# Kernel tuning notes

Measured on AMD Instinct MI355X. Metric: run time of the kernel, lower is better.

The kernel has to match this reference:

```python
import jax, jax.numpy as jnp
import numpy as np

N_NODES = 20000
N_EDGES = 60000
N_GRAPHS = 512
TOWERS = 4
F_OUT_T = 18  # out_channels // towers
HID = 72      # 8 * 9
EPS_BN = 1e-5
EPS_STD = 1e-5
DEG_HIST = np.array([67167, 3157428, 5106064, 885236, 453935, 0, 11152], dtype=np.float64)
AVG_DEG_LOG = float((np.log(np.arange(7) + 1.0) * DEG_HIST).sum() / DEG_HIST.sum())
UNITSCALE = jnp.array([[[1.0, 1.0, 100.0, 0.01, 1000.0, 0.0, 1e-5]]], dtype=jnp.float32)


def _lin(key, fan_in, fan_out, prefix=()):
    kw, kb = jax.random.split(key)
    s = 1.0 / np.sqrt(fan_in)
    w = jax.random.uniform(kw, prefix + (fan_in, fan_out), jnp.float32, -s, s)
    b = jax.random.uniform(kb, prefix + (fan_out,), jnp.float32, -s, s)
    return w, b


def setup_inputs() -> dict:
    key = jax.random.key(0)
    ks = list(jax.random.split(key, 32))
    it = iter(ks)
    nk = lambda: next(it)
    inp = {}
    inp['x'] = jax.random.normal(nk(), (N_NODES, 9), jnp.float32)
    inp['edge_attr'] = jax.random.normal(nk(), (N_EDGES, 3), jnp.float32)
    inp['edge_index'] = jax.random.randint(nk(), (2, N_EDGES), 0, N_NODES, jnp.int32)
    inp['batch'] = jnp.sort(jax.random.randint(nk(), (N_NODES,), 0, N_GRAPHS, jnp.int32))
    # conv layer 0: F_in = 9
    inp['c0_ew'], inp['c0_eb'] = _lin(nk(), 3, 9)
    inp['c0_prw'], inp['c0_prb'] = _lin(nk(), 27, 9, (TOWERS,))      # pre: 3*F_in -> F_in
    inp['c0_pow'], inp['c0_pob'] = _lin(nk(), 117, 18, (TOWERS,))   # post: 13*F_in -> 18
    inp['c0_lw'], inp['c0_lb'] = _lin(nk(), HID, HID)
    inp['c0_g'] = jnp.ones((HID,), jnp.float32)
    inp['c0_be'] = jnp.zeros((HID,), jnp.float32)
    # conv layers 1-3 stacked: F_in = 72
    inp['cs_ew'], inp['cs_eb'] = _lin(nk(), 3, HID, (3,))
    inp['cs_prw'], inp['cs_prb'] = _lin(nk(), 216, HID, (3, TOWERS))
    inp['cs_pow'], inp['cs_pob'] = _lin(nk(), 936, 18, (3, TOWERS))
    inp['cs_lw'], inp['cs_lb'] = _lin(nk(), HID, HID, (3,))
    inp['cs_g'] = jnp.ones((3, HID), jnp.float32)
    inp['cs_be'] = jnp.zeros((3, HID), jnp.float32)
    # MLP heads
    for m, out_d in (('m1', 3), ('m2', 7), ('m3', 7)):
        inp[m + '_w1'], inp[m + '_b1'] = _lin(nk(), HID, 50)
        inp[m + '_g1'] = jnp.ones((50,), jnp.float32)
        inp[m + '_be1'] = jnp.zeros((50,), jnp.float32)
        inp[m + '_w2'], inp[m + '_b2'] = _lin(nk(), 50, 25)
        inp[m + '_g2'] = jnp.ones((25,), jnp.float32)
        inp[m + '_be2'] = jnp.zeros((25,), jnp.float32)
        inp[m + '_w3'], inp[m + '_b3'] = _lin(nk(), 25, out_d)
    return inp


def _batchnorm(x, g, b):
    # training-mode BatchNorm1d (biased variance)
    mu = x.mean(axis=0)
    var = x.var(axis=0)
    return (x - mu) * jax.lax.rsqrt(var + EPS_BN) * g + b


def _pna_conv(x, src, dst, edge_attr, ew, eb, prw, prb, pow_, pob, lw, lb):
    n, f_in = x.shape
    e_enc = edge_attr @ ew + eb                                 # [E, F_in]
    h = jnp.concatenate([x[dst], x[src], e_enc], axis=-1)       # [E, 3*F_in]
    # per-tower pre-MLP (pre_layers=1 -> single Linear); input identical per tower
    msg = jnp.einsum('ef,tfo->eto', h, prw) + prb               # [E, T, F_in]

    deg = jax.ops.segment_sum(jnp.ones((src.shape[0],), jnp.float32), dst, n)  # in-degree [N]
    degc = jnp.maximum(deg, 1.0)[:, None, None]
    s1 = jax.ops.segment_sum(msg, dst, n)
    s2 = jax.ops.segment_sum(msg * msg, dst, n)
    mean = s1 / degc
    var = jax.nn.relu(s2 / degc - mean * mean)
    std = jnp.sqrt(var + EPS_STD)
    has = (deg > 0)[:, None, None]
    mn = jnp.where(has, jax.ops.segment_min(msg, dst, n), 0.0)
    mx = jnp.where(has, jax.ops.segment_max(msg, dst, n), 0.0)
    agg = jnp.concatenate([mean, mn, mx, std], axis=-1)         # [N, T, 4*F_in]

    amp = (jnp.log(jnp.maximum(deg, 1.0) + 1.0) / AVG_DEG_LOG)[:, None, None]
    out = jnp.concatenate([agg, agg * amp, agg / amp], axis=-1)  # identity/amplification/attenuation

    xt = jnp.broadcast_to(x[:, None, :], (n, TOWERS, f_in))
    comb = jnp.concatenate([xt, out], axis=-1)                  # [N, T, 13*F_in]
    o = jnp.einsum('ntf,tfo->nto', comb, pow_) + pob            # [N, T, 18]
    return o.reshape(n, TOWERS * F_OUT_T) @ lw + lb             # [N, 72]


def _mlp_head(x, w1, b1, g1, be1, w2, b2, g2, be2, w3, b3):
    h = jax.nn.relu(_batchnorm(x @ w1 + b1, g1, be1))
    h = jax.nn.relu(_batchnorm(h @ w2 + b2, g2, be2))
    return h @ w3 + b3


def _forward(x, edge_attr, edge_index, batch,
             c0_ew, c0_eb, c0_prw, c0_prb, c0_pow, c0_pob, c0_lw, c0_lb, c0_g, c0_be,
             cs_ew, cs_eb, cs_prw, cs_prb, cs_pow, cs_pob, cs_lw, cs_lb, cs_g, cs_be,
             m1_w1, m1_b1, m1_g1, m1_be1, m1_w2, m1_b2, m1_g2, m1_be2, m1_w3, m1_b3,
             m2_w1, m2_b1, m2_g1, m2_be1, m2_w2, m2_b2, m2_g2, m2_be2, m2_w3, m2_b3,
             m3_w1, m3_b1, m3_g1, m3_be1, m3_w2, m3_b2, m3_g2, m3_be2, m3_w3, m3_b3):
    src, dst = edge_index[0], edge_index[1]
    h = _pna_conv(x, src, dst, edge_attr, c0_ew, c0_eb, c0_prw, c0_prb, c0_pow, c0_pob, c0_lw, c0_lb)
    h = jax.nn.relu(_batchnorm(h, c0_g, c0_be))
    for i in range(3):
        h = _pna_conv(h, src, dst, edge_attr, cs_ew[i], cs_eb[i], cs_prw[i], cs_prb[i],
                      cs_pow[i], cs_pob[i], cs_lw[i], cs_lb[i])
        h = jax.nn.relu(_batchnorm(h, cs_g[i], cs_be[i]))
    g = jax.ops.segment_sum(h, batch, N_GRAPHS)                 # global_add_pool -> [G, 72]
    kij = jnp.tanh(_mlp_head(g, m1_w1, m1_b1, m1_g1, m1_be1, m1_w2, m1_b2, m1_g2, m1_be2, m1_w3, m1_b3))
    kij = jnp.broadcast_to(kij[:, None, :], (N_GRAPHS, 2, 3))
    c1 = jax.nn.relu(_mlp_head(g, m2_w1, m2_b1, m2_g1, m2_be1, m2_w2, m2_b2, m2_g2, m2_be2, m2_w3, m2_b3))[:, None, :]
    c2 = jax.nn.relu(_mlp_head(g, m3_w1, m3_b1, m3_g1, m3_be1, m3_w2, m3_b2, m3_g2, m3_be2, m3_w3, m3_b3))[:, None, :]
    out = jnp.concatenate([c1, c2], axis=1) + UNITSCALE         # [G, 2, 7]
    return jnp.concatenate([out, kij], axis=-1)                 # [G, 2, 10]


def reference(x, edge_attr, edge_index, batch,
              c0_ew, c0_eb, c0_prw, c0_prb, c0_pow, c0_pob, c0_lw, c0_lb, c0_g, c0_be,
              cs_ew, cs_eb, cs_prw, cs_prb, cs_pow, cs_pob, cs_lw, cs_lb, cs_g, cs_be,
              m1_w1, m1_b1, m1_g1, m1_be1, m1_w2, m1_b2, m1_g2, m1_be2, m1_w3, m1_b3,
              m2_w1, m2_b1, m2_g1, m2_be1, m2_w2, m2_b2, m2_g2, m2_be2, m2_w3, m2_b3,
              m3_w1, m3_b1, m3_g1, m3_be1, m3_w2, m3_b2, m3_g2, m3_be2, m3_w3, m3_b3):
    return _forward(x, edge_attr, edge_index, batch,
                    c0_ew, c0_eb, c0_prw, c0_prb, c0_pow, c0_pob, c0_lw, c0_lb, c0_g, c0_be,
                    cs_ew, cs_eb, cs_prw, cs_prb, cs_pow, cs_pob, cs_lw, cs_lb, cs_g, cs_be,
                    m1_w1, m1_b1, m1_g1, m1_be1, m1_w2, m1_b2, m1_g2, m1_be2, m1_w3, m1_b3,
                    m2_w1, m2_b1, m2_g1, m2_be1, m2_w2, m2_b2, m2_g2, m2_be2, m2_w3, m2_b3,
                    m3_w1, m3_b1, m3_g1, m3_be1, m3_w2, m3_b2, m3_g2, m3_be2, m3_w3, m3_b3)
```

## Files before the change

kernel.cpp:

```cpp
#include <hip/hip_runtime.h>
#include <math.h>
#include <cstdint>

#define N_NODES 20000
#define N_EDGES 60000
#define N_GRAPHS 512
#define NT 4

__global__ void count_deg_k(const int* __restrict__ dst, int* __restrict__ deg) {
  int e = blockIdx.x * blockDim.x + threadIdx.x;
  if (e < N_EDGES) atomicAdd(&deg[dst[e]], 1);
}

__global__ void scan_rowptr_k(const int* __restrict__ deg, int* __restrict__ rp) {
  __shared__ int ss[1024];
  int tid = threadIdx.x;
  const int per = (N_NODES + 1023) / 1024;
  int base = tid * per;
  int s = 0;
  for (int i = 0; i < per; i++) { int idx = base + i; if (idx < N_NODES) s += deg[idx]; }
  ss[tid] = s;
  __syncthreads();
  for (int off = 1; off < 1024; off <<= 1) {
    int v = (tid >= off) ? ss[tid - off] : 0;
    __syncthreads();
    ss[tid] += v;
    __syncthreads();
  }
  int run = ss[tid] - s;
  for (int i = 0; i < per; i++) {
    int idx = base + i;
    if (idx < N_NODES) { rp[idx] = run; run += deg[idx]; }
  }
  if (tid == 0) rp[N_NODES] = ss[1023];
}

__global__ void fill_csr_k(const int* __restrict__ dst, const int* __restrict__ rp,
                           int* __restrict__ cur, int* __restrict__ eids) {
  int e = blockIdx.x * blockDim.x + threadIdx.x;
  if (e < N_EDGES) {
    int d = dst[e];
    int pos = atomicAdd(&cur[d], 1);
    eids[rp[d] + pos] = e;
  }
}

__global__ void amp_k(const int* __restrict__ deg, float* __restrict__ amp, float adl) {
  int n = blockIdx.x * blockDim.x + threadIdx.x;
  if (n < N_NODES) {
    float d = (float)(deg[n] > 0 ? deg[n] : 1);
    amp[n] = logf(d + 1.0f) / adl;
  }
}

__global__ void gboundary_k(const int* __restrict__ batch, int* __restrict__ grp) {
  int n = blockIdx.x * blockDim.x + threadIdx.x;
  if (n >= N_NODES) return;
  int bn = batch[n];
  int bp = (n == 0) ? -1 : batch[n - 1];
  for (int g = bp + 1; g <= bn; g++) grp[g] = n;
  if (n == N_NODES - 1)
    for (int g = bn + 1; g <= N_GRAPHS; g++) grp[g] = N_NODES;
}

template <int AVEC, int BNA, int EPI>
__global__ __launch_bounds__(256, 2) void sgemm2_k(
    const float* __restrict__ A, const float* __restrict__ B, float* __restrict__ C,
    const float* __restrict__ bias, int M, int N, int K, int lda, int ldb, int ldc,
    int nb, int ns, long long bsA, long long bsB,
    const float* __restrict__ vsc, const float* __restrict__ vsh,
    const float* __restrict__ amp, float* __restrict__ y0, int ldy,
    double* __restrict__ bnsums) {
  constexpr int SM = (EPI == 1) ? 128 * 57 : (16 * 128 + 16 * 64);
  __shared__ float smem[SM];
  float(*As)[128] = (float(*)[128])smem;
  float(*Bs)[64] = (float(*)[64])(smem + 16 * 128);

  const int tid = threadIdx.x;
  const int tx = tid & 15, ty = tid >> 4;
  const int m0 = blockIdx.x * 128, n0 = blockIdx.y * 64;
  const int z = blockIdx.z;
  A += bsA * z; B += bsB * z;

  float acc[8][4] = {};
  for (int k0 = 0; k0 < K; k0 += 16) {
    if (AVEC) {
#pragma unroll
      for (int it = 0; it < 2; ++it) {
        int u = it * 256 + tid;
        int row = u >> 2, q = u & 3;
        int gm = m0 + row, gk = k0 + 4 * q;
        float4 v = make_float4(0.f, 0.f, 0.f, 0.f);
        if (gm < M && gk < K) {
          v = *(const float4*)&A[(long long)gm * lda + gk];
          if (BNA) {
            float4 sc = *(const float4*)&vsc[gk];
            float4 sh = *(const float4*)&vsh[gk];
            v.x = fmaxf(v.x * sc.x + sh.x, 0.f);
            v.y = fmaxf(v.y * sc.y + sh.y, 0.f);
            v.z = fmaxf(v.z * sc.z + sh.z, 0.f);
            v.w = fmaxf(v.w * sc.w + sh.w, 0.f);
          }
        }
        As[4 * q + 0][row] = v.x;
        As[4 * q + 1][row] = v.y;
        As[4 * q + 2][row] = v.z;
        As[4 * q + 3][row] = v.w;
      }
    } else {
#pragma unroll
      for (int it = 0; it < 8; ++it) {
        int u = it * 256 + tid;
        int row = u >> 4, kk = u & 15;
        int gm = m0 + row, gk = k0 + kk;
        float v = 0.f;
        if (gm < M && gk < K) {
          v = A[(long long)gm * lda + gk];
          if (BNA) v = fmaxf(v * vsc[gk] + vsh[gk], 0.f);
        }
        As[kk][row] = v;
      }
    }
    {
      int kk = tid >> 4, n4 = (tid & 15) * 4;
      int gk = k0 + kk, gn = n0 + n4;
      float4 v = make_float4(0.f, 0.f, 0.f, 0.f);
      if (gk < K && gn < nb) v = *(const float4*)&B[(long long)gk * ldb + gn];
      *(float4*)&Bs[kk][n4] = v;
    }
    __syncthreads();
#pragma unroll
    for (int kk = 0; kk < 16; ++kk) {
      float a[8], b[4];
#pragma unroll
      for (int i = 0; i < 8; i++) a[i] = As[kk][ty * 8 + i];
#pragma unroll
      for (int j = 0; j < 4; j++) b[j] = Bs[kk][tx * 4 + j];
#pragma unroll
      for (int i = 0; i < 8; i++)
#pragma unroll
        for (int j = 0; j < 4; j++) acc[i][j] += a[i] * b[j];
    }
    __syncthreads();
  }

  if (EPI == 1) {
    float(*Ps)[57] = (float(*)[57])smem;
    int c0 = tx * 4;
#pragma unroll
    for (int i = 0; i < 8; i++) {
      if (c0 < 56) {
#pragma unroll
        for (int j = 0; j < 4; j++) Ps[ty * 8 + i][c0 + j] = acc[i][j];
      }
    }
    __syncthreads();
#pragma unroll
    for (int it = 0; it < 9; ++it) {
      int item = it * 256 + tid;
      int r = item / 18, o = item - r * 18;
      int gm = m0 + r;
      if (gm < M) {
        float a = amp[gm];
        float v = Ps[r][o] + a * Ps[r][18 + o] + Ps[r][36 + o] / a;
        y0[(long long)gm * ldy + z * 18 + o] += v;
      }
    }
    return;
  }

  int gn = n0 + tx * 4;
  float cs[4] = {0.f, 0.f, 0.f, 0.f}, cq[4] = {0.f, 0.f, 0.f, 0.f};
  if (gn < ns) {
    float b0 = 0.f, b1 = 0.f, b2 = 0.f, b3 = 0.f;
    if (bias) { b0 = bias[gn]; b1 = bias[gn + 1]; b2 = bias[gn + 2]; b3 = bias[gn + 3]; }
#pragma unroll
    for (int i = 0; i < 8; i++) {
      int gm = m0 + ty * 8 + i;
      if (gm >= M) continue;
      float4 v;
      v.x = acc[i][0] + b0; v.y = acc[i][1] + b1;
      v.z = acc[i][2] + b2; v.w = acc[i][3] + b3;
      *(float4*)&C[(long long)gm * ldc + gn] = v;
      if (EPI == 2) {
        cs[0] += v.x; cs[1] += v.y; cs[2] += v.z; cs[3] += v.w;
        cq[0] += v.x * v.x; cq[1] += v.y * v.y; cq[2] += v.z * v.z; cq[3] += v.w * v.w;
      }
    }
  }
  if (EPI == 2) {
    __syncthreads();
    float* psum = smem;
    float* psq = smem + 1024;
#pragma unroll
    for (int j = 0; j < 4; j++) {
      psum[ty * 64 + tx * 4 + j] = cs[j];
      psq[ty * 64 + tx * 4 + j] = cq[j];
    }
    __syncthreads();
    if (tid < 64) {
      float s = 0.f, q = 0.f;
#pragma unroll
      for (int t = 0; t < 16; t++) { s += psum[t * 64 + tid]; q += psq[t * 64 + tid]; }
      int gcol = n0 + tid;
      if (gcol < N) {
        atomicAdd(&bnsums[gcol], (double)s);
        atomicAdd(&bnsums[72 + gcol], (double)q);
      }
    }
  }
}

__global__ void agg_fused_k(const float* __restrict__ XdXs, int ldx, const float* __restrict__ ea,
                            const int* __restrict__ srcI, const int* __restrict__ rp,
                            const int* __restrict__ eids, const float* __restrict__ Wec,
                            const float* __restrict__ bec, float* __restrict__ agg, int F) {
  const int C = 4 * F;
  long long idx = (long long)blockIdx.x * blockDim.x + threadIdx.x;
  if (idx >= (long long)N_NODES * C) return;
  int n = (int)(idx / C), c = (int)(idx % C);
  int s = rp[n], e = rp[n + 1];
  float w0 = Wec[c], w1 = Wec[C + c], w2 = Wec[2 * C + c], bc = bec[c];
  float sum = 0.f, sq = 0.f, mn = INFINITY, mx = -INFINITY;
  for (int i = s; i < e; i++) {
    int eid = eids[i];
    int sr = srcI[eid];
    float v = XdXs[(long long)sr * ldx + C + c] + ea[eid * 3 + 0] * w0 +
              ea[eid * 3 + 1] * w1 + ea[eid * 3 + 2] * w2 + bc;
    sum += v; sq += v * v;
    mn = fminf(mn, v); mx = fmaxf(mx, v);
  }
  int t = c / F, f = c % F;
  long long base = (long long)n * 4 * C + (long long)t * 4 * F;
  float mean, stdv;
  if (e == s) {
    mean = 0.f; mn = 0.f; mx = 0.f; stdv = sqrtf(1e-5f);
  } else {
    float inv = 1.f / (float)(e - s);
    float xd = XdXs[(long long)n * ldx + c];
    float mu = sum * inv;
    float var = sq * inv - mu * mu;
    if (var < 0.f) var = 0.f;
    stdv = sqrtf(var + 1e-5f);
    mean = xd + mu; mn += xd; mx += xd;
  }
  agg[base + f] = mean;
  agg[base + F + f] = mn;
  agg[base + 2 * F + f] = mx;
  agg[base + 3 * F + f] = stdv;
}

__global__ void repack2_k(const float* __restrict__ prw, const float* __restrict__ pw,
                          const float* __restrict__ ew, const float* __restrict__ eb,
                          const float* __restrict__ prb, const float* __restrict__ pob,
                          float* __restrict__ Bm, float* __restrict__ bfull,
                          float* __restrict__ Wc, float* __restrict__ Wec,
                          float* __restrict__ bec, int F) {
  const int C = 4 * F, F3 = 3 * F, F8 = 8 * F;
  const int Nfull = F8 + 72;
  const int nBm = F * Nfull, nbf = Nfull, nWc = 4 * C * 64, nWec = 3 * C, nbec = C;
  int idx = blockIdx.x * blockDim.x + threadIdx.x;
  if (idx < nBm) {
    int f = idx / Nfull, c = idx % Nfull;
    float v;
    if (c < F8) {
      int cc = (c < C) ? c : (c - C);
      int t = cc / F, o = cc % F;
      int row = (c < C) ? f : (F + f);
      v = prw[((long long)t * F3 + row) * F + o];
    } else {
      int c2 = c - F8;
      int t = c2 / 18, o = c2 % 18;
      v = pw[((long long)t * 13 * F + f) * 18 + o];
    }
    Bm[idx] = v;
  } else if (idx < nBm + nbf) {
    int c = idx - nBm;
    bfull[c] = (c < F8) ? 0.f : pob[c - F8];
  } else if (idx < nBm + nbf + nWc) {
    int j2 = idx - nBm - nbf;
    int t = j2 / (C * 64);
    int rem = j2 % (C * 64);
    int j = rem / 64, col = rem % 64;
    float v = 0.f;
    if (col < 54) {
      int seg = col / 18, o = col % 18;
      int row = (seg == 0) ? (F + j) : ((seg == 1) ? (5 * F + j) : (9 * F + j));
      v = pw[((long long)t * 13 * F + row) * 18 + o];
    }
    Wc[j2] = v;
  } else if (idx < nBm + nbf + nWc + nWec) {
    int j2 = idx - nBm - nbf - nWc;
    int r = j2 / C, c = j2 % C;
    int t = c / F, o = c % F;
    float s = 0.f;
    for (int f = 0; f < F; f++) s += ew[r * F + f] * prw[((long long)t * F3 + 2 * F + f) * F + o];
    Wec[j2] = s;
  } else if (idx < nBm + nbf + nWc + nWec + nbec) {
    int c = idx - (nBm + nbf + nWc + nWec);
    int t = c / F, o = c % F;
    float s = prb[t * F + o];
    for (int f = 0; f < F; f++) s += eb[f] * prw[((long long)t * F3 + 2 * F + f) * F + o];
    bec[c] = s;
  }
}

__global__ void bnfinal_k(const double* __restrict__ sums, const float* __restrict__ g,
                          const float* __restrict__ be, float* __restrict__ vsc,
                          float* __restrict__ vsh) {
  int c = threadIdx.x;
  if (c >= 72) return;
  double mu = sums[c] / (double)N_NODES;
  double var = sums[72 + c] / (double)N_NODES - mu * mu;
  if (var < 0.0) var = 0.0;
  float sc = g[c] / sqrtf((float)var + 1e-5f);
  vsc[c] = sc;
  vsh[c] = be[c] - (float)mu * sc;
}

__global__ __launch_bounds__(256) void pool2_k(const float* __restrict__ y,
                                               const float* __restrict__ vsc,
                                               const float* __restrict__ vsh,
                                               const int* __restrict__ grp,
                                               float* __restrict__ gpT) {
  int g = blockIdx.x;
  int s = grp[g], e = grp[g + 1];
  __shared__ float acc[72];
  if (threadIdx.x < 72) acc[threadIdx.x] = 0.f;
  __syncthreads();
  int tot = (e - s) * 72;
  for (int idx = threadIdx.x; idx < tot; idx += 256) {
    int n = s + idx / 72, c = idx % 72;
    float v = y[(long long)n * 72 + c] * vsc[c] + vsh[c];
    if (v > 0.f) atomicAdd(&acc[c], v);
  }
  __syncthreads();
  if (threadIdx.x < 72) gpT[threadIdx.x * N_GRAPHS + g] = acc[threadIdx.x];
}

struct HeadP {
  const float *w1, *b1, *g1, *be1, *w2, *b2, *g2, *be2, *w3, *b3;
};

__device__ inline float wred(float v) {
#pragma unroll
  for (int off = 32; off > 0; off >>= 1) v += __shfl_xor(v, off);
  return v;
}

__global__ __launch_bounds__(512) void head_l1_k(const float* __restrict__ gpT, HeadP hA,
                                                 HeadP hB, HeadP hC, float* __restrict__ h1T) {
  int head = blockIdx.x / 50, o = blockIdx.x % 50;
  HeadP hp = (head == 0) ? hA : ((head == 1) ? hB : hC);
  int r = threadIdx.x, lane = r & 63, wave = r >> 6;
  __shared__ float rs[8], rq[8], sc_sh, sh_sh;
  float acc = hp.b1[o];
  for (int k = 0; k < 72; k++) acc += gpT[k * N_GRAPHS + r] * hp.w1[k * 50 + o];
  float s = wred(acc), q = wred(acc * acc);
  if (lane == 0) { rs[wave] = s; rq[wave] = q; }
  __syncthreads();
  if (r == 0) {
    float ts = 0.f, tq = 0.f;
#pragma unroll
    for (int i = 0; i < 8; i++) { ts += rs[i]; tq += rq[i]; }
    float mu = ts / (float)N_GRAPHS;
    float var = tq / (float)N_GRAPHS - mu * mu;
    if (var < 0.f) var = 0.f;
    float sc = hp.g1[o] / sqrtf(var + 1e-5f);
    sc_sh = sc; sh_sh = hp.be1[o] - mu * sc;
  }
  __syncthreads();
  float v = acc * sc_sh + sh_sh;
  h1T[(head * 50 + o) * N_GRAPHS + r] = v > 0.f ? v : 0.f;
}

__global__ __launch_bounds__(512) void head_l2_k(const float* __restrict__ h1T, HeadP hA,
                                                 HeadP hB, HeadP hC, float* __restrict__ h2T) {
  int head = blockIdx.x / 25, o = blockIdx.x % 25;
  HeadP hp = (head == 0) ? hA : ((head == 1) ? hB : hC);
  int r = threadIdx.x, lane = r & 63, wave = r >> 6;
  __shared__ float rs[8], rq[8], sc_sh, sh_sh;
  float acc = hp.b2[o];
  const float* hb = h1T + head * 50 * N_GRAPHS;
  for (int k = 0; k < 50; k++) acc += hb[k * N_GRAPHS + r] * hp.w2[k * 25 + o];
  float s = wred(acc), q = wred(acc * acc);
  if (lane == 0) { rs[wave] = s; rq[wave] = q; }
  __syncthreads();
  if (r == 0) {
    float ts = 0.f, tq = 0.f;
#pragma unroll
    for (int i = 0; i < 8; i++) { ts += rs[i]; tq += rq[i]; }
    float mu = ts / (float)N_GRAPHS;
    float var = tq / (float)N_GRAPHS - mu * mu;
    if (var < 0.f) var = 0.f;
    float sc = hp.g2[o] / sqrtf(var + 1e-5f);
    sc_sh = sc; sh_sh = hp.be2[o] - mu * sc;
  }
  __syncthreads();
  float v = acc * sc_sh + sh_sh;
  h2T[(head * 25 + o) * N_GRAPHS + r] = v > 0.f ? v : 0.f;
}

__global__ __launch_bounds__(512) void head_l3_k(const float* __restrict__ h2T, HeadP hA,
                                                 HeadP hB, HeadP hC, float* __restrict__ out) {
  int head = blockIdx.x;
  HeadP hp = (head == 0) ? hA : ((head == 1) ? hB : hC);
  int r = threadIdx.x;
  int od = (head == 0) ? 3 : 7;
  float acc3[7];
#pragma unroll
  for (int o = 0; o < 7; o++) acc3[o] = (o < od) ? hp.b3[o] : 0.f;
  const float* hb = h2T + head * 25 * N_GRAPHS;
  for (int k = 0; k < 25; k++) {
    float hv = hb[k * N_GRAPHS + r];
#pragma unroll
    for (int o = 0; o < 7; o++)
      if (o < od) acc3[o] += hv * hp.w3[k * od + o];
  }
  float* og = out + r * 20;
  if (head == 0) {
#pragma unroll
    for (int j = 0; j < 3; j++) {
      float v = tanhf(acc3[j]);
      og[7 + j] = v;
      og[17 + j] = v;
    }
  } else {
    const float unit[7] = {1.f, 1.f, 100.f, 0.01f, 1000.f, 0.f, 1e-5f};
    int base = (head == 1) ? 0 : 10;
#pragma unroll
    for (int j = 0; j < 7; j++) {
      float v = acc3[j];
      v = v > 0.f ? v : 0.f;
      og[base + j] = v + unit[j];
    }
  }
}

static inline char* alignp(char* p, size_t a) {
  return (char*)(((uintptr_t)p + (a - 1)) & ~(uintptr_t)(a - 1));
}

extern "C" void kernel_launch(void* const* d_in, const int* in_sizes, int n_in, void* d_out,
                              int out_size, void* d_ws, size_t ws_size, hipStream_t stream) {
  const float* x = (const float*)d_in[0];
  const float* edge_attr = (const float*)d_in[1];
  const int* srcp = (const int*)d_in[2];
  const int* dstp = srcp + N_EDGES;
  const int* batch = (const int*)d_in[3];

  const float *EWv[4], *EBv[4], *PRW[4], *PRB[4], *PW[4], *POB[4], *LWv[4], *LBv[4], *Gv[4],
      *BEv[4];
  EWv[0] = (const float*)d_in[4];  EBv[0] = (const float*)d_in[5];
  PRW[0] = (const float*)d_in[6];  PRB[0] = (const float*)d_in[7];
  PW[0] = (const float*)d_in[8];   POB[0] = (const float*)d_in[9];
  LWv[0] = (const float*)d_in[10]; LBv[0] = (const float*)d_in[11];
  Gv[0] = (const float*)d_in[12];  BEv[0] = (const float*)d_in[13];
  const float* cs_ew = (const float*)d_in[14];
  const float* cs_eb = (const float*)d_in[15];
  const float* cs_prw = (const float*)d_in[16];
  const float* cs_prb = (const float*)d_in[17];
  const float* cs_pow = (const float*)d_in[18];
  const float* cs_pob = (const float*)d_in[19];
  const float* cs_lw = (const float*)d_in[20];
  const float* cs_lb = (const float*)d_in[21];
  const float* cs_g = (const float*)d_in[22];
  const float* cs_be = (const float*)d_in[23];
  for (int i = 1; i < 4; i++) {
    int j = i - 1;
    EWv[i] = cs_ew + j * 3 * 72;        EBv[i] = cs_eb + j * 72;
    PRW[i] = cs_prw + j * 4 * 216 * 72; PRB[i] = cs_prb + j * 4 * 72;
    PW[i] = cs_pow + j * 4 * 936 * 18;  POB[i] = cs_pob + j * 4 * 18;
    LWv[i] = cs_lw + j * 72 * 72;       LBv[i] = cs_lb + j * 72;
    Gv[i] = cs_g + j * 72;              BEv[i] = cs_be + j * 72;
  }
  HeadP heads[3];
  for (int m = 0; m < 3; m++) {
    const float** pp = (const float**)&heads[m];
    for (int k = 0; k < 10; k++) pp[k] = (const float*)d_in[24 + m * 10 + k];
  }

  char* p = (char*)d_ws;
  int* deg_i = (int*)p;   p += N_NODES * 4;
  int* cursor = (int*)p;  p += N_NODES * 4;
  int* row_ptr = (int*)p; p += (N_NODES + 1) * 4;
  int* eids = (int*)p;    p += N_EDGES * 4;
  int* grp = (int*)p;     p += (N_GRAPHS + 1) * 4;
  p = alignp(p, 256);
  float* amp = (float*)p; p += N_NODES * 4;
  p = alignp(p, 256);
  float* R = (float*)p;   p += (size_t)N_NODES * 648 * 4;
  p = alignp(p, 256);
  float* y1 = (float*)p;  p += (size_t)N_NODES * 72 * 4;
  p = alignp(p, 256);
  float* agg = (float*)p; p += (size_t)N_NODES * 1152 * 4;
  p = alignp(p, 256);
  float* Bm = (float*)p;    p += 72 * 648 * 4;
  float* bfull = (float*)p; p += 648 * 4;
  float* Wc = (float*)p;    p += 4 * 288 * 64 * 4;
  float* Wec = (float*)p;   p += 3 * 288 * 4;
  float* bec = (float*)p;   p += 288 * 4;
  float* vsc = (float*)p;   p += 72 * 4;
  float* vsh = (float*)p;   p += 72 * 4;
  p = alignp(p, 256);
  double* bnsums = (double*)p; p += 144 * 8;
  p = alignp(p, 256);
  float* gpT = (float*)p;  p += 72 * N_GRAPHS * 4;
  float* h1T = (float*)p;  p += 3 * 50 * N_GRAPHS * 4;
  float* h2T = (float*)p;  p += 3 * 25 * N_GRAPHS * 4;
  (void)ws_size; (void)n_in; (void)in_sizes; (void)out_size;

  static const double hist[7] = {67167, 3157428, 5106064, 885236, 453935, 0, 11152};
  double num = 0, den = 0;
  for (int i = 0; i < 7; i++) { num += log((double)(i + 1)) * hist[i]; den += hist[i]; }
  float adl = (float)(num / den);

  hipMemsetAsync(deg_i, 0, 2 * N_NODES * 4, stream);
  count_deg_k<<<(N_EDGES + 255) / 256, 256, 0, stream>>>(dstp, deg_i);
  scan_rowptr_k<<<1, 1024, 0, stream>>>(deg_i, row_ptr);
  fill_csr_k<<<(N_EDGES + 255) / 256, 256, 0, stream>>>(dstp, row_ptr, cursor, eids);
  amp_k<<<(N_NODES + 255) / 256, 256, 0, stream>>>(deg_i, amp, adl);
  gboundary_k<<<(N_NODES + 255) / 256, 256, 0, stream>>>(batch, grp);

  const int gM = (N_NODES + 127) / 128;
  for (int l = 0; l < 4; l++) {
    const int F = (l == 0) ? 9 : 72;
    const int C = 4 * F, Nfull = 8 * F + 72;
    float* y0l = R + 8 * F;

    int nrep = F * Nfull + Nfull + 4 * C * 64 + 3 * C + C;
    repack2_k<<<(nrep + 255) / 256, 256, 0, stream>>>(PRW[l], PW[l], EWv[l], EBv[l], PRB[l],
                                                      POB[l], Bm, bfull, Wc, Wec, bec, F);
    hipMemsetAsync(bnsums, 0, 144 * 8, stream);

    {
      dim3 g(gM, (Nfull + 63) / 64, 1);
      if (l == 0)
        sgemm2_k<0, 0, 0><<<g, 256, 0, stream>>>(x, Bm, R, bfull, N_NODES, Nfull, F, F, Nfull,
                                                 Nfull, Nfull, Nfull, 0, 0, nullptr, nullptr,
                                                 nullptr, nullptr, 0, nullptr);
      else
        sgemm2_k<1, 1, 0><<<g, 256, 0, stream>>>(y1, Bm, R, bfull, N_NODES, Nfull, F, 72, Nfull,
                                                 Nfull, Nfull, Nfull, 0, 0, vsc, vsh, nullptr,
                                                 nullptr, 0, nullptr);
    }

    {
      long long tot = (long long)N_NODES * C;
      agg_fused_k<<<(int)((tot + 255) / 256), 256, 0, stream>>>(R, Nfull, edge_attr, srcp,
                                                                row_ptr, eids, Wec, bec, agg, F);
    }

    {
      dim3 g(gM, 1, 4);
      sgemm2_k<1, 0, 1><<<g, 256, 0, stream>>>(agg, Wc, nullptr, nullptr, N_NODES, 54, C, 4 * C,
                                               64, 0, 64, 56, C, (long long)C * 64, nullptr,
                                               nullptr, amp, y0l, Nfull, nullptr);
    }

    {
      dim3 g(gM, 2, 1);
      sgemm2_k<1, 0, 2><<<g, 256, 0, stream>>>(y0l, LWv[l], y1, LBv[l], N_NODES, 72, 72, Nfull,
                                               72, 72, 72, 72, 0, 0, nullptr, nullptr, nullptr,
                                               nullptr, 0, bnsums);
    }

    bnfinal_k<<<1, 128, 0, stream>>>(bnsums, Gv[l], BEv[l], vsc, vsh);
  }

  pool2_k<<<N_GRAPHS, 256, 0, stream>>>(y1, vsc, vsh, grp, gpT);

  head_l1_k<<<150, 512, 0, stream>>>(gpT, heads[0], heads[1], heads[2], h1T);
  head_l2_k<<<75, 512, 0, stream>>>(h1T, heads[0], heads[1], heads[2], h2T);
  head_l3_k<<<3, 512, 0, stream>>>(h2T, heads[0], heads[1], heads[2], (float*)d_out);
}
```

Baseline: 940.9 us.

## Move node GEMMs to split-bf16 MFMA with hi/lo operand decomposition

Replaces the FP32 SIMT sgemm for the pre-transform GEMM and the tower post GEMM with an MFMA kernel that splits each operand into bf16 high and low parts and accumulates three products to approximate FP32 accuracy. The aggregation kernel now writes hi/lo bf16 planes directly in a K-padded layout, and new conversion kernels pre-split x and the BN+ReLU-normalized activations. Weights are repacked transposed and split. This adds extra conversion passes and memsets, and trades exact FP32 for near-FP32 split-bf16 precision.

```diff
diff --git a/kernel.cpp b/kernel.cpp
--- a/kernel.cpp
+++ b/kernel.cpp
@@ -1,4 +1,5 @@
 #include <hip/hip_runtime.h>
+#include <hip/hip_bf16.h>
 #include <math.h>
 #include <cstdint>
 
@@ -6,6 +7,22 @@
 #define N_EDGES 60000
 #define N_GRAPHS 512
 #define NT 4
+
+typedef __attribute__((ext_vector_type(8))) short bf8v;
+typedef __attribute__((ext_vector_type(4))) float f4v;
+
+__device__ inline unsigned short bf_rn(float a) {
+  unsigned int x = __float_as_uint(a);
+  unsigned int lsb = (x >> 16) & 1u;
+  x += 0x7fffu + lsb;
+  return (unsigned short)(x >> 16);
+}
+__device__ inline void bsplit(float a, unsigned short& h, unsigned short& l) {
+  unsigned short hu = bf_rn(a);
+  float hf = __uint_as_float(((unsigned int)hu) << 16);
+  h = hu;
+  l = bf_rn(a - hf);
+}
 
 __global__ void count_deg_k(const int* __restrict__ dst, int* __restrict__ deg) {
   int e = blockIdx.x * blockDim.x + threadIdx.x;
@@ -61,6 +78,152 @@
   for (int g = bp + 1; g <= bn; g++) grp[g] = n;
   if (n == N_NODES - 1)
     for (int g = bn + 1; g <= N_GRAPHS; g++) grp[g] = N_NODES;
+}
+
+__global__ void cvt_x_k(const float* __restrict__ x, unsigned short* __restrict__ xh,
+                        unsigned short* __restrict__ xl) {
+  int idx = blockIdx.x * blockDim.x + threadIdx.x;
+  if (idx >= N_NODES * 32) return;
+  int n = idx >> 5, k = idx & 31;
+  float a = (k < 9) ? x[n * 9 + k] : 0.f;
+  bsplit(a, xh[idx], xl[idx]);
+}
+
+__global__ void cvt_act_k(const float* __restrict__ y1, const float* __restrict__ vsc,
+                          const float* __restrict__ vsh, unsigned short* __restrict__ ah,
+                          unsigned short* __restrict__ al) {
+  int idx = blockIdx.x * blockDim.x + threadIdx.x;
+  if (idx >= N_NODES * 96) return;
+  int n = idx / 96, k = idx - n * 96;
+  float a = 0.f;
+  if (k < 72) {
+    a = y1[n * 72 + k] * vsc[k] + vsh[k];
+    if (a < 0.f) a = 0.f;
+  }
+  bsplit(a, ah[idx], al[idx]);
+}
+
+template <int EPI>
+__global__ __launch_bounds__(256, 2) void mgemm_k(
+    const unsigned short* __restrict__ Ah, const unsigned short* __restrict__ Al,
+    const unsigned short* __restrict__ Bh, const unsigned short* __restrict__ Bl,
+    float* __restrict__ C, const float* __restrict__ bias, int M, int N, int Kp, int lda,
+    int ldb, int ldc, long long bsA, long long bsB, const float* __restrict__ amp,
+    float* __restrict__ y0, int ldy) {
+  __shared__ __align__(16) unsigned short smem[15360];
+  unsigned short* sAh = smem;
+  unsigned short* sAl = smem + 5120;
+  unsigned short* sBh = smem + 10240;
+  unsigned short* sBl = smem + 12800;
+
+  const int tid = threadIdx.x;
+  const int lane = tid & 63, wid = tid >> 6;
+  const int wm = wid >> 1, wn = wid & 1;
+  const int lrow = lane & 15, lko = (lane >> 4) * 8;
+  const int m0 = blockIdx.x * 128, n0 = blockIdx.y * 64;
+  const int z = blockIdx.z;
+  Ah += bsA * z; Al += bsA * z; Bh += bsB * z; Bl += bsB * z;
+
+  f4v acc[4][2];
+#pragma unroll
+  for (int i = 0; i < 4; i++)
+#pragma unroll
+    for (int j = 0; j < 2; j++) acc[i][j] = (f4v){0.f, 0.f, 0.f, 0.f};
+
+  const uint4 zero4 = make_uint4(0, 0, 0, 0);
+  for (int k0 = 0; k0 < Kp; k0 += 32) {
+#pragma unroll
+    for (int it = 0; it < 2; ++it) {
+      int u = it * 256 + tid;
+      int row = u >> 2, ch = u & 3;
+      int gm = m0 + row;
+      uint4 vh = zero4, vl = zero4;
+      if (gm < M) {
+        long long go = (long long)gm * lda + k0 + ch * 8;
+        vh = *(const uint4*)&Ah[go];
+        vl = *(const uint4*)&Al[go];
+      }
+      *(uint4*)&sAh[row * 40 + ch * 8] = vh;
+      *(uint4*)&sAl[row * 40 + ch * 8] = vl;
+    }
+    {
+      int col = tid >> 2, ch = tid & 3;
+      int gn = n0 + col;
+      uint4 vh = zero4, vl = zero4;
+      if (gn < N) {
+        long long go = (long long)gn * ldb + k0 + ch * 8;
+        vh = *(const uint4*)&Bh[go];
+        vl = *(const uint4*)&Bl[go];
+      }
+      *(uint4*)&sBh[col * 40 + ch * 8] = vh;
+      *(uint4*)&sBl[col * 40 + ch * 8] = vl;
+    }
+    __syncthreads();
+    bf8v bhv[2], blv[2];
+#pragma unroll
+    for (int ni = 0; ni < 2; ++ni) {
+      int cb = (wn * 32 + ni * 16 + lrow) * 40 + lko;
+      bhv[ni] = *(const bf8v*)&sBh[cb];
+      blv[ni] = *(const bf8v*)&sBl[cb];
+    }
+#pragma unroll
+    for (int mi = 0; mi < 4; ++mi) {
+      int ab = (wm * 64 + mi * 16 + lrow) * 40 + lko;
+      bf8v ahv = *(const bf8v*)&sAh[ab];
+      bf8v alv = *(const bf8v*)&sAl[ab];
+#pragma unroll
+      for (int ni = 0; ni < 2; ++ni) {
+        acc[mi][ni] = __builtin_amdgcn_mfma_f32_16x16x32_bf16(ahv, bhv[ni], acc[mi][ni], 0, 0, 0);
+        acc[mi][ni] = __builtin_amdgcn_mfma_f32_16x16x32_bf16(ahv, blv[ni], acc[mi][ni], 0, 0, 0);
+        acc[mi][ni] = __builtin_amdgcn_mfma_f32_16x16x32_bf16(alv, bhv[ni], acc[mi][ni], 0, 0, 0);
+      }
+    }
+    __syncthreads();
+  }
+
+  if (EPI == 1) {
+    float* Ps = (float*)smem;
+#pragma unroll
+    for (int mi = 0; mi < 4; ++mi)
+#pragma unroll
+      for (int ni = 0; ni < 2; ++ni) {
+        int col = wn * 32 + ni * 16 + lrow;
+        if (col < 56) {
+#pragma unroll
+          for (int r = 0; r < 4; ++r) {
+            int row = wm * 64 + mi * 16 + ((lane >> 4) << 2) + r;
+            Ps[row * 57 + col] = acc[mi][ni][r];
+          }
+        }
+      }
+    __syncthreads();
+#pragma unroll
+    for (int it = 0; it < 9; ++it) {
+      int item = it * 256 + tid;
+      int r = item / 18, o = item - r * 18;
+      int gm = m0 + r;
+      if (gm < M) {
+        float a = amp[gm];
+        float v = Ps[r * 57 + o] + a * Ps[r * 57 + 18 + o] + Ps[r * 57 + 36 + o] / a;
+        y0[(long long)gm * ldy + z * 18 + o] += v;
+      }
+    }
+    return;
+  }
+#pragma unroll
+  for (int ni = 0; ni < 2; ++ni) {
+    int col = n0 + wn * 32 + ni * 16 + lrow;
+    if (col >= N) continue;
+    float bv = bias ? bias[col] : 0.f;
+#pragma unroll
+    for (int mi = 0; mi < 4; ++mi) {
+#pragma unroll
+      for (int r = 0; r < 4; ++r) {
+        int row = m0 + wm * 64 + mi * 16 + ((lane >> 4) << 2) + r;
+        if (row < M) C[(long long)row * ldc + col] = acc[mi][ni][r] + bv;
+      }
+    }
+  }
 }
 
 template <int AVEC, int BNA, int EPI>
@@ -214,7 +377,8 @@
 __global__ void agg_fused_k(const float* __restrict__ XdXs, int ldx, const float* __restrict__ ea,
                             const int* __restrict__ srcI, const int* __restrict__ rp,
                             const int* __restrict__ eids, const float* __restrict__ Wec,
-                            const float* __restrict__ bec, float* __restrict__ agg, int F) {
+                            const float* __restrict__ bec, unsigned short* __restrict__ aggh,
+                            unsigned short* __restrict__ aggl, int F, int Kpz) {
   const int C = 4 * F;
   long long idx = (long long)blockIdx.x * blockDim.x + threadIdx.x;
   if (idx >= (long long)N_NODES * C) return;
@@ -231,7 +395,6 @@
     mn = fminf(mn, v); mx = fmaxf(mx, v);
   }
   int t = c / F, f = c % F;
-  long long base = (long long)n * 4 * C + (long long)t * 4 * F;
   float mean, stdv;
   if (e == s) {
     mean = 0.f; mn = 0.f; mx = 0.f; stdv = sqrtf(1e-5f);
@@ -244,60 +407,65 @@
     stdv = sqrtf(var + 1e-5f);
     mean = xd + mu; mn += xd; mx += xd;
   }
-  agg[base + f] = mean;
-  agg[base + F + f] = mn;
-  agg[base + 2 * F + f] = mx;
-  agg[base + 3 * F + f] = stdv;
-}
-
-__global__ void repack2_k(const float* __restrict__ prw, const float* __restrict__ pw,
+  long long base = (long long)n * 4 * Kpz + (long long)t * Kpz;
+  bsplit(mean, aggh[base + f], aggl[base + f]);
+  bsplit(mn, aggh[base + F + f], aggl[base + F + f]);
+  bsplit(mx, aggh[base + 2 * F + f], aggl[base + 2 * F + f]);
+  bsplit(stdv, aggh[base + 3 * F + f], aggl[base + 3 * F + f]);
+}
+
+__global__ void repack3_k(const float* __restrict__ prw, const float* __restrict__ pw,
                           const float* __restrict__ ew, const float* __restrict__ eb,
                           const float* __restrict__ prb, const float* __restrict__ pob,
-                          float* __restrict__ Bm, float* __restrict__ bfull,
-                          float* __restrict__ Wc, float* __restrict__ Wec,
-                          float* __restrict__ bec, int F) {
+                          unsigned short* __restrict__ BmTh, unsigned short* __restrict__ BmTl,
+                          float* __restrict__ bfull, unsigned short* __restrict__ WcTh,
+                          unsigned short* __restrict__ WcTl, float* __restrict__ Wec,
+                          float* __restrict__ bec, int F, int KpA, int KpW) {
   const int C = 4 * F, F3 = 3 * F, F8 = 8 * F;
   const int Nfull = F8 + 72;
-  const int nBm = F * Nfull, nbf = Nfull, nWc = 4 * C * 64, nWec = 3 * C, nbec = C;
+  const int nBmT = Nfull * KpA, nbf = Nfull, nWcT = 4 * 64 * KpW, nWec = 3 * C, nbec = C;
   int idx = blockIdx.x * blockDim.x + threadIdx.x;
-  if (idx < nBm) {
-    int f = idx / Nfull, c = idx % Nfull;
-    float v;
-    if (c < F8) {
-      int cc = (c < C) ? c : (c - C);
-      int t = cc / F, o = cc % F;
-      int row = (c < C) ? f : (F + f);
-      v = prw[((long long)t * F3 + row) * F + o];
-    } else {
-      int c2 = c - F8;
-      int t = c2 / 18, o = c2 % 18;
-      v = pw[((long long)t * 13 * F + f) * 18 + o];
-    }
-    Bm[idx] = v;
-  } else if (idx < nBm + nbf) {
-    int c = idx - nBm;
+  if (idx < nBmT) {
+    int c = idx / KpA, k = idx % KpA;
+    float v = 0.f;
+    if (k < F) {
+      int f = k;
+      if (c < F8) {
+        int cc = (c < C) ? c : (c - C);
+        int t = cc / F, o = cc % F;
+        int row = (c < C) ? f : (F + f);
+        v = prw[((long long)t * F3 + row) * F + o];
+      } else {
+        int c2 = c - F8;
+        int t = c2 / 18, o = c2 % 18;
+        v = pw[((long long)t * 13 * F + f) * 18 + o];
+      }
+    }
+    bsplit(v, BmTh[idx], BmTl[idx]);
+  } else if (idx < nBmT + nbf) {
+    int c = idx - nBmT;
     bfull[c] = (c < F8) ? 0.f : pob[c - F8];
-  } else if (idx < nBm + nbf + nWc) {
-    int j2 = idx - nBm - nbf;
-    int t = j2 / (C * 64);
-    int rem = j2 % (C * 64);
-    int j = rem / 64, col = rem % 64;
+  } else if (idx < nBmT + nbf + nWcT) {
+    int j = idx - nBmT - nbf;
+    int t = j / (64 * KpW);
+    int rem = j % (64 * KpW);
+    int col = rem / KpW, k = rem % KpW;
     float v = 0.f;
-    if (col < 54) {
+    if (col < 54 && k < C) {
       int seg = col / 18, o = col % 18;
-      int row = (seg == 0) ? (F + j) : ((seg == 1) ? (5 * F + j) : (9 * F + j));
+      int row = (seg == 0) ? (F + k) : ((seg == 1) ? (5 * F + k) : (9 * F + k));
       v = pw[((long long)t * 13 * F + row) * 18 + o];
     }
-    Wc[j2] = v;
-  } else if (idx < nBm + nbf + nWc + nWec) {
-    int j2 = idx - nBm - nbf - nWc;
+    bsplit(v, WcTh[j], WcTl[j]);
+  } else if (idx < nBmT + nbf + nWcT + nWec) {
+    int j2 = idx - nBmT - nbf - nWcT;
     int r = j2 / C, c = j2 % C;
     int t = c / F, o = c % F;
     float s = 0.f;
     for (int f = 0; f < F; f++) s += ew[r * F + f] * prw[((long long)t * F3 + 2 * F + f) * F + o];
     Wec[j2] = s;
-  } else if (idx < nBm + nbf + nWc + nWec + nbec) {
-    int c = idx - (nBm + nbf + nWc + nWec);
+  } else if (idx < nBmT + nbf + nWcT + nWec + nbec) {
+    int c = idx - (nBmT + nbf + nWcT + nWec);
     int t = c / F, o = c % F;
     float s = prb[t * F + o];
     for (int f = 0; f < F; f++) s += eb[f] * prw[((long long)t * F3 + 2 * F + f) * F + o];
@@ -493,11 +661,20 @@
   p = alignp(p, 256);
   float* y1 = (float*)p;  p += (size_t)N_NODES * 72 * 4;
   p = alignp(p, 256);
-  float* agg = (float*)p; p += (size_t)N_NODES * 1152 * 4;
-  p = alignp(p, 256);
-  float* Bm = (float*)p;    p += 72 * 648 * 4;
+  unsigned short* aggh = (unsigned short*)p; p += (size_t)N_NODES * 1152 * 2;
+  unsigned short* aggl = (unsigned short*)p; p += (size_t)N_NODES * 1152 * 2;
+  p = alignp(p, 256);
+  unsigned short* xh = (unsigned short*)p;   p += (size_t)N_NODES * 32 * 2;
+  unsigned short* xl = (unsigned short*)p;   p += (size_t)N_NODES * 32 * 2;
+  unsigned short* acth = (unsigned short*)p; p += (size_t)N_NODES * 96 * 2;
+  unsigned short* actl = (unsigned short*)p; p += (size_t)N_NODES * 96 * 2;
+  p = alignp(p, 256);
+  unsigned short* BmTh = (unsigned short*)p; p += 648 * 96 * 2;
+  unsigned short* BmTl = (unsigned short*)p; p += 648 * 96 * 2;
+  unsigned short* WcTh = (unsigned short*)p; p += 4 * 64 * 288 * 2;
+  unsigned short* WcTl = (unsigned short*)p; p += 4 * 64 * 288 * 2;
+  p = alignp(p, 256);
   float* bfull = (float*)p; p += 648 * 4;
-  float* Wc = (float*)p;    p += 4 * 288 * 64 * 4;
   float* Wec = (float*)p;   p += 3 * 288 * 4;
   float* bec = (float*)p;   p += 288 * 4;
   float* vsc = (float*)p;   p += 72 * 4;
@@ -521,41 +698,43 @@
   fill_csr_k<<<(N_EDGES + 255) / 256, 256, 0, stream>>>(dstp, row_ptr, cursor, eids);
   amp_k<<<(N_NODES + 255) / 256, 256, 0, stream>>>(deg_i, amp, adl);
   gboundary_k<<<(N_NODES + 255) / 256, 256, 0, stream>>>(batch, grp);
+  cvt_x_k<<<(N_NODES * 32 + 255) / 256, 256, 0, stream>>>(x, xh, xl);
+  hipMemsetAsync(aggh, 0, (size_t)N_NODES * 256 * 2, stream);
+  hipMemsetAsync(aggl, 0, (size_t)N_NODES * 256 * 2, stream);
 
   const int gM = (N_NODES + 127) / 128;
   for (int l = 0; l < 4; l++) {
     const int F = (l == 0) ? 9 : 72;
     const int C = 4 * F, Nfull = 8 * F + 72;
+    const int KpA = (l == 0) ? 32 : 96;
+    const int Kpz = (l == 0) ? 64 : 288;
     float* y0l = R + 8 * F;
 
-    int nrep = F * Nfull + Nfull + 4 * C * 64 + 3 * C + C;
-    repack2_k<<<(nrep + 255) / 256, 256, 0, stream>>>(PRW[l], PW[l], EWv[l], EBv[l], PRB[l],
-                                                      POB[l], Bm, bfull, Wc, Wec, bec, F);
+    int nrep = Nfull * KpA + Nfull + 4 * 64 * Kpz + 3 * C + C;
+    repack3_k<<<(nrep + 255) / 256, 256, 0, stream>>>(PRW[l], PW[l], EWv[l], EBv[l], PRB[l],
+                                                      POB[l], BmTh, BmTl, bfull, WcTh, WcTl,
+                                                      Wec, bec, F, KpA, Kpz);
     hipMemsetAsync(bnsums, 0, 144 * 8, stream);
 
     {
       dim3 g(gM, (Nfull + 63) / 64, 1);
-      if (l == 0)
-        sgemm2_k<0, 0, 0><<<g, 256, 0, stream>>>(x, Bm, R, bfull, N_NODES, Nfull, F, F, Nfull,
-                                                 Nfull, Nfull, Nfull, 0, 0, nullptr, nullptr,
-                                                 nullptr, nullptr, 0, nullptr);
-      else
-        sgemm2_k<1, 1, 0><<<g, 256, 0, stream>>>(y1, Bm, R, bfull, N_NODES, Nfull, F, 72, Nfull,
-                                                 Nfull, Nfull, Nfull, 0, 0, vsc, vsh, nullptr,
-                                                 nullptr, 0, nullptr);
+      mgemm_k<0><<<g, 256, 0, stream>>>((l == 0) ? xh : acth, (l == 0) ? xl : actl, BmTh, BmTl,
+                                        R, bfull, N_NODES, Nfull, KpA, KpA, KpA, Nfull, 0, 0,
+                                        nullptr, nullptr, 0);
     }
 
     {
       long long tot = (long long)N_NODES * C;
       agg_fused_k<<<(int)((tot + 255) / 256), 256, 0, stream>>>(R, Nfull, edge_attr, srcp,
-                                                                row_ptr, eids, Wec, bec, agg, F);
+                                                                row_ptr, eids, Wec, bec, aggh,
+                                                                aggl, F, Kpz);
     }
 
     {
       dim3 g(gM, 1, 4);
-      sgemm2_k<1, 0, 1><<<g, 256, 0, stream>>>(agg, Wc, nullptr, nullptr, N_NODES, 54, C, 4 * C,
-                                               64, 0, 64, 56, C, (long long)C * 64, nullptr,
-                                               nullptr, amp, y0l, Nfull, nullptr);
+      mgemm_k<1><<<g, 256, 0, stream>>>(aggh, aggl, WcTh, WcTl, nullptr, nullptr, N_NODES, 64,
+                                        Kpz, 4 * Kpz, Kpz, 0, Kpz, (long long)64 * Kpz, amp,
+                                        y0l, Nfull);
     }
 
     {
@@ -566,6 +745,9 @@
     }
 
     bnfinal_k<<<1, 128, 0, stream>>>(bnsums, Gv[l], BEv[l], vsc, vsh);
+
+    if (l < 3)
+      cvt_act_k<<<(N_NODES * 96 + 255) / 256, 256, 0, stream>>>(y1, vsc, vsh, acth, actl);
   }
 
   pool2_k<<<N_GRAPHS, 256, 0, stream>>>(y1, vsc, vsh, grp, gpT);
```

New measurement: 882.8 us. 6.2% less time.
